# Optimization experiments

Measured on AMD Instinct MI355X. Metric: run time of the kernel, lower is better.

The kernel has to match this reference:

```python
import jax, jax.numpy as jnp
import numpy as np

B, T, E, H, L = 8, 4096, 1024, 16, 64  # batch, seq, embed, heads, local window
HD = E // H


def setup_inputs() -> dict:
    key = jax.random.key(0)
    ks = jax.random.split(key, 5)
    s = 1.0 / np.sqrt(E).astype(np.float32)
    x = jax.random.normal(ks[0], (B, T, E), dtype=jnp.float32)
    W_qkv = jax.random.normal(ks[1], (3 * E, E), dtype=jnp.float32) * s
    b_qkv = jnp.zeros((3 * E,), dtype=jnp.float32)
    W_out = jax.random.normal(ks[2], (E, E), dtype=jnp.float32) * s
    b_out = jnp.zeros((E,), dtype=jnp.float32)
    return {"x": x, "W_qkv": W_qkv, "b_qkv": b_qkv, "W_out": W_out, "b_out": b_out}


def reference(x, W_qkv, b_qkv, W_out, b_out):
    b, t, e = x.shape
    scaling = HD ** (-0.5)
    # T is already a multiple of L, so need_pad = 0 (matches torch path)
    qkv = x @ W_qkv.T + b_qkv                      # (B,T,3E)
    q, k, v = jnp.split(qkv, 3, axis=-1)           # each (B,T,E)
    q = q * scaling

    def to_blocks(a):
        # (B,T,E) -> (B,H,T/L,L,HD); matches torch view/transpose sequence
        return a.reshape(b, t, H, HD).transpose(0, 2, 1, 3).reshape(b, H, t // L, L, HD)

    qb, kb, vb = to_blocks(q), to_blocks(k), to_blocks(v)
    attn = jax.nn.softmax(jnp.einsum('bhnld,bhnmd->bhnlm', qb, kb), axis=-1)
    out = jnp.einsum('bhnlm,bhnmd->bhnld', attn, vb)  # (B,H,N,L,HD)
    out = out.reshape(b, H, t, HD).transpose(0, 2, 1, 3).reshape(b, t, e)
    return out @ W_out.T + b_out
```

## Files before the change

kernel.cpp:

```cpp
#include <hip/hip_runtime.h>
#include <hip/hip_bf16.h>

typedef __hip_bfloat16 bf16;
typedef __attribute__((ext_vector_type(8))) short short8;
typedef __attribute__((ext_vector_type(4))) float f32x4;

__device__ __forceinline__ void gload_lds16(const void* g, void* l) {
    __builtin_amdgcn_global_load_lds(
        (const __attribute__((address_space(1))) void*)g,
        (__attribute__((address_space(3))) void*)l, 16, 0, 0);
}

__device__ __forceinline__ void store_out(bf16* p, float v)  { *p = __float2bfloat16(v); }
__device__ __forceinline__ void store_out(float* p, float v) { *p = v; }

__global__ __launch_bounds__(256)
void cvt_f32_bf16(const float* __restrict__ in, bf16* __restrict__ out, long n)
{
    const long i = ((long)blockIdx.x * 256 + threadIdx.x) * 8;
    if (i + 8 > n) return;
    float4 a = *(const float4*)(in + i);
    float4 b = *(const float4*)(in + i + 4);
    bf16 o[8];
    o[0] = __float2bfloat16(a.x); o[1] = __float2bfloat16(a.y);
    o[2] = __float2bfloat16(a.z); o[3] = __float2bfloat16(a.w);
    o[4] = __float2bfloat16(b.x); o[5] = __float2bfloat16(b.y);
    o[6] = __float2bfloat16(b.z); o[7] = __float2bfloat16(b.w);
    *(uint4*)(out + i) = *(const uint4*)o;
}

template <typename OutT>
__global__ __launch_bounds__(256)
void gemm_bt_bias(const bf16* __restrict__ A, const bf16* __restrict__ Bt,
                  const float* __restrict__ bias, OutT* __restrict__ C,
                  int N, int K)
{
    __shared__ bf16 As[128 * 32];
    __shared__ bf16 Bs[128 * 32];

    const int tid = threadIdx.x;
    const int wv  = tid >> 6;
    const int ln  = tid & 63;
    const int l15 = ln & 15;
    const int qd  = ln >> 4;
    const int wm  = wv >> 1, wn = wv & 1;
    const long m0 = (long)blockIdx.y * 128;
    const long n0 = (long)blockIdx.x * 128;

    const int e0 = tid * 8;
    const int e1 = (256 + tid) * 8;
    const int ar0 = e0 >> 5, ac0 = e0 & 31;
    const int ar1 = e1 >> 5, ac1 = e1 & 31;
    bf16* lA0 = &As[wv * 512];
    bf16* lA1 = &As[2048 + wv * 512];
    bf16* lB0 = &Bs[wv * 512];
    bf16* lB1 = &Bs[2048 + wv * 512];

    f32x4 acc[4][4] = {};

    for (int k0 = 0; k0 < K; k0 += 32) {
        gload_lds16(A  + (m0 + ar0) * K + k0 + ac0, lA0);
        gload_lds16(A  + (m0 + ar1) * K + k0 + ac1, lA1);
        gload_lds16(Bt + (n0 + ar0) * K + k0 + ac0, lB0);
        gload_lds16(Bt + (n0 + ar1) * K + k0 + ac1, lB1);
        __syncthreads();

        short8 af[4], bfr[4];
#pragma unroll
        for (int mi = 0; mi < 4; ++mi)
            af[mi] = *(const short8*)&As[(wm * 64 + mi * 16 + l15) * 32 + qd * 8];
#pragma unroll
        for (int ni = 0; ni < 4; ++ni)
            bfr[ni] = *(const short8*)&Bs[(wn * 64 + ni * 16 + l15) * 32 + qd * 8];
#pragma unroll
        for (int mi = 0; mi < 4; ++mi)
#pragma unroll
            for (int ni = 0; ni < 4; ++ni)
                acc[mi][ni] = __builtin_amdgcn_mfma_f32_16x16x32_bf16(
                    af[mi], bfr[ni], acc[mi][ni], 0, 0, 0);
        __syncthreads();
    }

    const long ccol = n0 + wn * 64;
    float bsv[4];
#pragma unroll
    for (int ni = 0; ni < 4; ++ni)
        bsv[ni] = bias[ccol + ni * 16 + l15];
#pragma unroll
    for (int mi = 0; mi < 4; ++mi) {
#pragma unroll
        for (int r = 0; r < 4; ++r) {
            const long row = m0 + wm * 64 + mi * 16 + qd * 4 + r;
            OutT* cp = C + row * N + ccol + l15;
#pragma unroll
            for (int ni = 0; ni < 4; ++ni)
                store_out(cp + ni * 16, acc[mi][ni][r] + bsv[ni]);
        }
    }
}

#define LROW 72

__global__ __launch_bounds__(256)
void attn_local(const bf16* __restrict__ qkv, bf16* __restrict__ out)
{
    __shared__ bf16 Qs[64 * LROW];
    __shared__ bf16 Ks[64 * LROW];
    __shared__ bf16 Vt[64 * LROW];
    __shared__ bf16 Ps[64 * LROW];

    const int cb = blockIdx.x;
    const int h  = blockIdx.y;
    const int tid = threadIdx.x;

    const long qoff = (long)cb * 64 * 3072 + h * 64;

#pragma unroll
    for (int p = 0; p < 2; ++p) {
        const int e = (p * 256 + tid) * 8;
        const int tk = e >> 6, cl = e & 63;
        const long g = qoff + (long)tk * 3072 + cl;
        *(uint4*)&Qs[tk * LROW + cl] = *(const uint4*)&qkv[g];
        *(uint4*)&Ks[tk * LROW + cl] = *(const uint4*)&qkv[g + 1024];
        uint4 vv = *(const uint4*)&qkv[g + 2048];
        const bf16* vp = (const bf16*)&vv;
#pragma unroll
        for (int j = 0; j < 8; ++j)
            Vt[(cl + j) * LROW + tk] = vp[j];
    }
    __syncthreads();

    const int wv = tid >> 6, ln = tid & 63, l15 = ln & 15, qd = ln >> 4;

    f32x4 sacc[4] = {};
#pragma unroll
    for (int kk = 0; kk < 64; kk += 32) {
        short8 aq = *(const short8*)&Qs[(wv * 16 + l15) * LROW + kk + qd * 8];
#pragma unroll
        for (int ni = 0; ni < 4; ++ni) {
            short8 bk = *(const short8*)&Ks[(ni * 16 + l15) * LROW + kk + qd * 8];
            sacc[ni] = __builtin_amdgcn_mfma_f32_16x16x32_bf16(aq, bk, sacc[ni], 0, 0, 0);
        }
    }

    float linv[4];
#pragma unroll
    for (int r = 0; r < 4; ++r) {
        float m = -3.4e38f;
#pragma unroll
        for (int ni = 0; ni < 4; ++ni) m = fmaxf(m, sacc[ni][r]);
#pragma unroll
        for (int off = 1; off < 16; off <<= 1) m = fmaxf(m, __shfl_xor(m, off));
        float s = 0.f, pv[4];
#pragma unroll
        for (int ni = 0; ni < 4; ++ni) {
            pv[ni] = __expf(0.125f * (sacc[ni][r] - m));
            s += pv[ni];
        }
#pragma unroll
        for (int off = 1; off < 16; off <<= 1) s += __shfl_xor(s, off);
        linv[r] = 1.f / s;
        const int row = wv * 16 + qd * 4 + r;
#pragma unroll
        for (int ni = 0; ni < 4; ++ni)
            Ps[row * LROW + ni * 16 + l15] = __float2bfloat16(pv[ni]);
    }
    __syncthreads();

    f32x4 oacc[4] = {};
#pragma unroll
    for (int kk = 0; kk < 64; kk += 32) {
        short8 ap = *(const short8*)&Ps[(wv * 16 + l15) * LROW + kk + qd * 8];
#pragma unroll
        for (int ni = 0; ni < 4; ++ni) {
            short8 bv = *(const short8*)&Vt[(ni * 16 + l15) * LROW + kk + qd * 8];
            oacc[ni] = __builtin_amdgcn_mfma_f32_16x16x32_bf16(ap, bv, oacc[ni], 0, 0, 0);
        }
    }

    const long obase = (long)cb * 64 * 1024 + h * 64;
#pragma unroll
    for (int r = 0; r < 4; ++r) {
        const int row = wv * 16 + qd * 4 + r;
#pragma unroll
        for (int ni = 0; ni < 4; ++ni)
            out[obase + (long)row * 1024 + ni * 16 + l15] =
                __float2bfloat16(oacc[ni][r] * linv[r]);
    }
}

extern "C" void kernel_launch(void* const* d_in, const int* in_sizes, int n_in,
                              void* d_out, int out_size, void* d_ws, size_t ws_size,
                              hipStream_t stream) {
    const float* x     = (const float*)d_in[0];
    const float* W_qkv = (const float*)d_in[1];
    const float* b_qkv = (const float*)d_in[2];
    const float* W_out = (const float*)d_in[3];
    const float* b_out = (const float*)d_in[4];
    float* out = (float*)d_out;

    bf16* Wqkv_b = (bf16*)d_ws;
    bf16* Wout_b = Wqkv_b + (size_t)3072 * 1024;
    bf16* chunk0 = Wout_b + (size_t)1024 * 1024;
    const size_t fixed_bytes = ((size_t)3072 * 1024 + (size_t)1024 * 1024) * 2;

    static const int cands[9] = {32768, 16384, 8192, 4096, 2048, 1024, 512, 256, 128};
    int CH = 128;
    for (int i = 0; i < 9; ++i)
        if (fixed_bytes + (size_t)cands[i] * 10240 <= ws_size) { CH = cands[i]; break; }

    bf16* xb    = chunk0;
    bf16* qkvb  = xb + (size_t)CH * 1024;
    bf16* attnb = qkvb + (size_t)CH * 3072;

    const dim3 blk(256);

    cvt_f32_bf16<<<dim3((3072 * 1024) / 2048), blk, 0, stream>>>(W_qkv, Wqkv_b, 3072 * 1024);
    cvt_f32_bf16<<<dim3((1024 * 1024) / 2048), blk, 0, stream>>>(W_out, Wout_b, 1024 * 1024);

    for (int c0 = 0; c0 < 32768; c0 += CH) {
        const long ne = (long)CH * 1024;
        cvt_f32_bf16<<<dim3((int)(ne / 2048)), blk, 0, stream>>>(x + (size_t)c0 * 1024, xb, ne);
        gemm_bt_bias<bf16><<<dim3(3072 / 128, CH / 128), blk, 0, stream>>>(
            xb, Wqkv_b, b_qkv, qkvb, 3072, 1024);
        attn_local<<<dim3(CH / 64, 16), blk, 0, stream>>>(qkvb, attnb);
        gemm_bt_bias<float><<<dim3(1024 / 128, CH / 128), blk, 0, stream>>>(
            attnb, Wout_b, b_out, out + (size_t)c0 * 1024, 1024, 1024);
    }
}
```

Measured before the change: 653.8 us.

## Replace GEMM with 256x256 tile, 4-stage LDS pipeline and XCD-aware block remap

The 128x128 single-buffered GEMM is replaced with a 512-thread, 256x256-tile kernel. It uses a 4-deep LDS ring of async global-to-LDS loads, with vmcnt waits and one barrier per k-step. Loads for the next stages are interleaved with the MFMA phases, and s_setprio raises priority around the math. Workgroup IDs are remapped so that consecutive tiles land on the same XCD for better L2 reuse. The larger tiles cut redundant global loads and barrier stalls, at the cost of more LDS (128KB per block) and registers, fewer blocks per chunk, and a minimum chunk size of 256 rows.

```diff
diff --git a/kernel.cpp b/kernel.cpp
--- a/kernel.cpp
+++ b/kernel.cpp
@@ -30,56 +30,101 @@
 }
 
 template <typename OutT>
-__global__ __launch_bounds__(256)
-void gemm_bt_bias(const bf16* __restrict__ A, const bf16* __restrict__ Bt,
-                  const float* __restrict__ bias, OutT* __restrict__ C,
-                  int N, int K)
+__global__ __launch_bounds__(512, 2)
+void gemm256(const bf16* __restrict__ A, const bf16* __restrict__ Bt,
+             const float* __restrict__ bias, OutT* __restrict__ C,
+             int N, int K, int gxt)
 {
-    __shared__ bf16 As[128 * 32];
-    __shared__ bf16 Bs[128 * 32];
+    __shared__ bf16 As[4][8192];
+    __shared__ bf16 Bs[4][8192];
+
+    const int nwg  = gridDim.x;
+    const int orig = blockIdx.x;
+    const int qq = nwg >> 3, rr = nwg & 7, xc = orig & 7;
+    const int wg = (xc < rr ? xc * (qq + 1) : rr * (qq + 1) + (xc - rr) * qq)
+                 + (orig >> 3);
+    const long m0 = (long)(wg / gxt) * 256;
+    const long n0 = (long)(wg % gxt) * 256;
 
     const int tid = threadIdx.x;
     const int wv  = tid >> 6;
     const int ln  = tid & 63;
     const int l15 = ln & 15;
     const int qd  = ln >> 4;
-    const int wm  = wv >> 1, wn = wv & 1;
-    const long m0 = (long)blockIdx.y * 128;
-    const long n0 = (long)blockIdx.x * 128;
+    const int wm  = wv >> 2, wn = wv & 3;
 
     const int e0 = tid * 8;
-    const int e1 = (256 + tid) * 8;
-    const int ar0 = e0 >> 5, ac0 = e0 & 31;
-    const int ar1 = e1 >> 5, ac1 = e1 & 31;
-    bf16* lA0 = &As[wv * 512];
-    bf16* lA1 = &As[2048 + wv * 512];
-    bf16* lB0 = &Bs[wv * 512];
-    bf16* lB1 = &Bs[2048 + wv * 512];
-
-    f32x4 acc[4][4] = {};
-
-    for (int k0 = 0; k0 < K; k0 += 32) {
-        gload_lds16(A  + (m0 + ar0) * K + k0 + ac0, lA0);
-        gload_lds16(A  + (m0 + ar1) * K + k0 + ac1, lA1);
-        gload_lds16(Bt + (n0 + ar0) * K + k0 + ac0, lB0);
-        gload_lds16(Bt + (n0 + ar1) * K + k0 + ac1, lB1);
-        __syncthreads();
-
-        short8 af[4], bfr[4];
-#pragma unroll
-        for (int mi = 0; mi < 4; ++mi)
-            af[mi] = *(const short8*)&As[(wm * 64 + mi * 16 + l15) * 32 + qd * 8];
+    const int r0 = e0 >> 5, c0 = e0 & 31;
+    const bf16* gA0 = A  + (m0 + r0) * K + c0;
+    const bf16* gA1 = A  + (m0 + 128 + r0) * K + c0;
+    const bf16* gB0 = Bt + (n0 + r0) * K + c0;
+    const bf16* gB1 = Bt + (n0 + 128 + r0) * K + c0;
+    const int lw = wv * 512;
+
+    const int NT = K >> 5;
+
+#define STAGE_A(bb, src) do { \
+        gload_lds16(gA0 + (src) * 32, &As[bb][lw]); \
+        gload_lds16(gA1 + (src) * 32, &As[bb][4096 + lw]); } while (0)
+#define STAGE_B(bb, src) do { \
+        gload_lds16(gB0 + (src) * 32, &Bs[bb][lw]); \
+        gload_lds16(gB1 + (src) * 32, &Bs[bb][4096 + lw]); } while (0)
+
+    {
+        const int s1 = 1 < NT ? 1 : 0;
+        const int s2 = 2 < NT ? 2 : 0;
+        STAGE_A(0, 0);  STAGE_B(0, 0);
+        STAGE_A(1, s1); STAGE_B(1, s1);
+        STAGE_A(2, s2); STAGE_B(2, s2);
+    }
+
+    f32x4 acc[8][4] = {};
+
+    for (int kt = 0; kt < NT; ++kt) {
+        const int b   = kt & 3;
+        const int ks  = kt + 3;
+        const int bb  = ks & 3;
+        const int src = ks < NT ? ks : 0;
+
+        asm volatile("s_waitcnt vmcnt(8)" ::: "memory");
+        __builtin_amdgcn_s_barrier();
+        asm volatile("" ::: "memory");
+
+        const bf16* Ab = As[b];
+        const bf16* Bb = Bs[b];
+
+        short8 af[4], bf[4];
+#pragma unroll
+        for (int mi = 0; mi < 4; ++mi)
+            af[mi] = *(const short8*)&Ab[(wm * 128 + mi * 16 + l15) * 32 + qd * 8];
 #pragma unroll
         for (int ni = 0; ni < 4; ++ni)
-            bfr[ni] = *(const short8*)&Bs[(wn * 64 + ni * 16 + l15) * 32 + qd * 8];
+            bf[ni] = *(const short8*)&Bb[(wn * 64 + ni * 16 + l15) * 32 + qd * 8];
+        STAGE_A(bb, src);
+        __builtin_amdgcn_s_setprio(1);
 #pragma unroll
         for (int mi = 0; mi < 4; ++mi)
 #pragma unroll
             for (int ni = 0; ni < 4; ++ni)
                 acc[mi][ni] = __builtin_amdgcn_mfma_f32_16x16x32_bf16(
-                    af[mi], bfr[ni], acc[mi][ni], 0, 0, 0);
-        __syncthreads();
-    }
+                    af[mi], bf[ni], acc[mi][ni], 0, 0, 0);
+        __builtin_amdgcn_s_setprio(0);
+
+#pragma unroll
+        for (int mi = 0; mi < 4; ++mi)
+            af[mi] = *(const short8*)&Ab[(wm * 128 + (mi + 4) * 16 + l15) * 32 + qd * 8];
+        STAGE_B(bb, src);
+        __builtin_amdgcn_s_setprio(1);
+#pragma unroll
+        for (int mi = 0; mi < 4; ++mi)
+#pragma unroll
+            for (int ni = 0; ni < 4; ++ni)
+                acc[mi + 4][ni] = __builtin_amdgcn_mfma_f32_16x16x32_bf16(
+                    af[mi], bf[ni], acc[mi + 4][ni], 0, 0, 0);
+        __builtin_amdgcn_s_setprio(0);
+    }
+#undef STAGE_A
+#undef STAGE_B
 
     const long ccol = n0 + wn * 64;
     float bsv[4];
@@ -87,10 +132,10 @@
     for (int ni = 0; ni < 4; ++ni)
         bsv[ni] = bias[ccol + ni * 16 + l15];
 #pragma unroll
-    for (int mi = 0; mi < 4; ++mi) {
+    for (int mi = 0; mi < 8; ++mi) {
 #pragma unroll
         for (int r = 0; r < 4; ++r) {
-            const long row = m0 + wm * 64 + mi * 16 + qd * 4 + r;
+            const long row = m0 + wm * 128 + mi * 16 + qd * 4 + r;
             OutT* cp = C + row * N + ccol + l15;
 #pragma unroll
             for (int ni = 0; ni < 4; ++ni)
@@ -204,9 +249,9 @@
     bf16* chunk0 = Wout_b + (size_t)1024 * 1024;
     const size_t fixed_bytes = ((size_t)3072 * 1024 + (size_t)1024 * 1024) * 2;
 
-    static const int cands[9] = {32768, 16384, 8192, 4096, 2048, 1024, 512, 256, 128};
-    int CH = 128;
-    for (int i = 0; i < 9; ++i)
+    static const int cands[8] = {32768, 16384, 8192, 4096, 2048, 1024, 512, 256};
+    int CH = 256;
+    for (int i = 0; i < 8; ++i)
         if (fixed_bytes + (size_t)cands[i] * 10240 <= ws_size) { CH = cands[i]; break; }
 
     bf16* xb    = chunk0;
@@ -214,17 +259,20 @@
     bf16* attnb = qkvb + (size_t)CH * 3072;
 
     const dim3 blk(256);
+    const dim3 gblk(512);
 
     cvt_f32_bf16<<<dim3((3072 * 1024) / 2048), blk, 0, stream>>>(W_qkv, Wqkv_b, 3072 * 1024);
     cvt_f32_bf16<<<dim3((1024 * 1024) / 2048), blk, 0, stream>>>(W_out, Wout_b, 1024 * 1024);
+
+    const int mt = CH / 256;
 
     for (int c0 = 0; c0 < 32768; c0 += CH) {
         const long ne = (long)CH * 1024;
         cvt_f32_bf16<<<dim3((int)(ne / 2048)), blk, 0, stream>>>(x + (size_t)c0 * 1024, xb, ne);
-        gemm_bt_bias<bf16><<<dim3(3072 / 128, CH / 128), blk, 0, stream>>>(
-            xb, Wqkv_b, b_qkv, qkvb, 3072, 1024);
+        gemm256<bf16><<<dim3(mt * (3072 / 256)), gblk, 0, stream>>>(
+            xb, Wqkv_b, b_qkv, qkvb, 3072, 1024, 3072 / 256);
         attn_local<<<dim3(CH / 64, 16), blk, 0, stream>>>(qkvb, attnb);
-        gemm_bt_bias<float><<<dim3(1024 / 128, CH / 128), blk, 0, stream>>>(
-            attnb, Wout_b, b_out, out + (size_t)c0 * 1024, 1024, 1024);
-    }
-}
+        gemm256<float><<<dim3(mt * (1024 / 256)), gblk, 0, stream>>>(
+            attnb, Wout_b, b_out, out + (size_t)c0 * 1024, 1024, 1024, 1024 / 256);
+    }
+}
```

Measured after the change: 576.6 us. 11.8% less time.
